# Optimization experiments

Hardware: AMD Instinct MI355X
Metric: run time of the kernel (lower is better)

Reference implementation:

```python
import jax, jax.numpy as jnp
import numpy as np

N = 8192   # points
C = 64     # feature planes (planes[0])
H = 4      # num_heads
K = 16     # nsample (KNN neighbors)
DH = C // H
EPS = 1e-9


def setup_inputs() -> dict:
    key = jax.random.key(0)
    ks = jax.random.split(key, 13)
    w = lambda k, sh: jax.random.normal(k, sh, jnp.float32) * 0.05
    p = jax.random.normal(ks[0], (N, 3), jnp.float32)
    nrm = jax.random.normal(ks[1], (N, 3), jnp.float32)
    normals = nrm / jnp.sqrt(jnp.sum(nrm * nrm, -1, keepdims=True) + EPS)
    x = jax.random.normal(ks[2], (N, C), jnp.float32)
    return {
        "p": p, "x": x, "normals": normals,
        "Wq": w(ks[3], (C, C)), "Wk": w(ks[4], (C, C)), "Wv": w(ks[5], (C, C)),
        "Wo": w(ks[6], (C, C)),
        "ppf_w1": w(ks[7], (4, C)), "ppf_b1": jnp.zeros((C,), jnp.float32),
        "ppf_w2": w(ks[8], (C, C)), "ppf_b2": jnp.zeros((C,), jnp.float32),
        "ln_g": jnp.ones((C,), jnp.float32), "ln_b": jnp.zeros((C,), jnp.float32),
    }


def _angle(u, v):
    # rotation-invariant angle via atan2(||u x v||, u . v); eps keeps grads finite at 0
    cr = jnp.cross(u, v)
    return jnp.arctan2(jnp.sqrt(jnp.sum(cr * cr, -1) + EPS), jnp.sum(u * v, -1))


def reference(p, x, normals, Wq, Wk, Wv, Wo, ppf_w1, ppf_b1, ppf_w2, ppf_b2, ln_g, ln_b):
    # --- KNN grouping (pointops.queryandgroup equivalent) ---
    sq = jnp.sum(p * p, -1)
    d2 = sq[:, None] + sq[None, :] - 2.0 * (p @ p.T)   # (N,N) pairwise sq dists
    _, idx = jax.lax.top_k(-d2, K)                      # (N,K) neighbor indices

    # --- PPF features (calc_ppf_gpu) ---
    p_r = p[idx]                                        # (N,K,3)
    n_r = normals[idx]                                  # (N,K,3)
    d = p_r - p[:, None, :]
    nc = jnp.broadcast_to(normals[:, None, :], d.shape)
    ppf = jnp.stack([
        _angle(nc, d),
        _angle(n_r, d),
        _angle(nc, n_r),
        jnp.sqrt(jnp.sum(d * d, -1) + EPS),
    ], -1)                                              # (N,K,4)

    # --- LocalPPFTransformer: PPF-conditioned local multi-head attention ---
    pe = jax.nn.relu(ppf @ ppf_w1 + ppf_b1) @ ppf_w2 + ppf_b2   # (N,K,C)
    q = (x @ Wq).reshape(N, H, DH)
    xg = x[idx]                                                  # (N,K,C) gather
    k = (xg @ Wk + pe).reshape(N, K, H, DH)
    v = (xg @ Wv + pe).reshape(N, K, H, DH)
    scale = 1.0 / np.sqrt(DH).astype(np.float32)
    attn = jax.nn.softmax(jnp.einsum('nhd,nkhd->nhk', q, k) * scale, axis=-1)
    out = jnp.einsum('nhk,nkhd->nhd', attn, v).reshape(N, C) @ Wo

    # --- block tail: LayerNorm, residual, ReLU ---
    mu = jnp.mean(out, -1, keepdims=True)
    var = jnp.var(out, -1, keepdims=True)
    out = (out - mu) * jax.lax.rsqrt(var + 1e-5) * ln_g + ln_b
    return jax.nn.relu(out + x)
```

## Files before the change

kernel.cpp:

```cpp
#include <hip/hip_runtime.h>
#include <hip/hip_bf16.h>
#include <math.h>

#define N_PTS 8192
#define QPW 4
#define LCAP 192
#define KNN_BLOCKS (N_PTS / 4)

#define OFF_W2 0
#define OFF_WO 4096
#define OFF_WQB 8192
#define OFF_WKB 12288
#define OFF_WVB 16384
#define PACK_N 20480
#define PREP_BLOCKS (N_PTS / 256)
#define PACK_BLOCKS ((PACK_N + 255) / 256)

typedef __hip_bfloat16 bf16;
typedef __attribute__((ext_vector_type(8))) short short8;
typedef __attribute__((ext_vector_type(4))) float floatx4;

#define INFF __int_as_float(0x7f800000)

__device__ __forceinline__ float ldf(const float* p, int i) { return p[i]; }
__device__ __forceinline__ float ldf(const bf16* p, int i) { return __bfloat162float(p[i]); }
__device__ __forceinline__ void stf(float* p, int i, float v) { p[i] = v; }
__device__ __forceinline__ void stf(bf16* p, int i, float v) { p[i] = __float2bfloat16(v); }

__device__ __forceinline__ unsigned short f2bfbits(float x) {
    bf16 h = __float2bfloat16(x);
    return *reinterpret_cast<unsigned short*>(&h);
}
__device__ __forceinline__ float bfbits2f(unsigned short u) {
    bf16 h;
    *reinterpret_cast<unsigned short*>(&h) = u;
    return __bfloat162float(h);
}

__device__ __forceinline__ short8 load_xfrag(const bf16* x, int row, int off) {
    return *(const short8*)((const unsigned short*)x + row * 64 + off);
}
__device__ __forceinline__ short8 load_xfrag(const float* x, int row, int off) {
    short8 v;
#pragma unroll
    for (int i = 0; i < 8; ++i) v[i] = (short)f2bfbits(x[row * 64 + off + i]);
    return v;
}

__device__ __forceinline__ bool is_bf16(const void* g) {
    return *(const unsigned int*)g != 0x3F800000u;
}

template <typename T>
__device__ __forceinline__ void prep_pack_body(const T* p, float4* p4,
                                               const T* w2, const T* Wo,
                                               const T* Wq, const T* Wk,
                                               const T* Wv,
                                               unsigned short* pack) {
    if (blockIdx.x < PREP_BLOCKS) {
        int i = blockIdx.x * 256 + threadIdx.x;
        float x = ldf(p, 3 * i + 0);
        float y = ldf(p, 3 * i + 1);
        float z = ldf(p, 3 * i + 2);
        p4[i] = make_float4(x, y, z, 0.5f * (x * x + y * y + z * z));
        return;
    }
    int i = (blockIdx.x - PREP_BLOCKS) * 256 + threadIdx.x;
    if (i >= PACK_N) return;
    if (i >= OFF_WO && i < OFF_WQB) {
        int j = i - OFF_WO, t = j >> 6, c = j & 63;
        pack[i] = f2bfbits(ldf(Wo, c * 64 + t));
    } else {
        const T* W = (i < OFF_WO) ? w2
                     : (i < OFF_WKB ? Wq : (i < OFF_WVB ? Wk : Wv));
        int j = i & 4095;
        int ii = j & 7, lane = (j >> 3) & 63, frag = j >> 9;
        int tile = frag >> 1, s = frag & 1, g = lane >> 4, m16 = lane & 15;
        int k = s * 32 + g * 8 + ii, n = tile * 16 + m16;
        pack[i] = f2bfbits(ldf(W, k * 64 + n));
    }
}
__global__ __launch_bounds__(256) void prep_pack_kernel(
    const void* p, float4* p4, const void* w2, const void* Wo, const void* Wq,
    const void* Wk, const void* Wv, unsigned short* pack, const void* gref) {
    if (is_bf16(gref))
        prep_pack_body<bf16>((const bf16*)p, p4, (const bf16*)w2,
                             (const bf16*)Wo, (const bf16*)Wq, (const bf16*)Wk,
                             (const bf16*)Wv, pack);
    else
        prep_pack_body<float>((const float*)p, p4, (const float*)w2,
                              (const float*)Wo, (const float*)Wq,
                              (const float*)Wk, (const float*)Wv, pack);
}

__device__ __forceinline__ float angle3(float ux, float uy, float uz, float vx,
                                        float vy, float vz) {
    float cx = uy * vz - uz * vy;
    float cy = uz * vx - ux * vz;
    float cz = ux * vy - uy * vx;
    float cn = sqrtf(cx * cx + cy * cy + cz * cz + 1e-9f);
    float d = ux * vx + uy * vy + uz * vz;
    return atan2f(cn, d);
}

template <typename T>
__device__ __forceinline__ void attn4_body(
    int n, int t, const float4* p4, const T* normals, const T* w1, const T* b1,
    const T* b2, const unsigned short* pack, const T* x, const T* ln_g,
    const T* ln_b, T* out, const int* nbr, float* scr,
    unsigned short (*kh)[72], unsigned short (*vbuf)[72]) {
    const int m16 = t & 15, g = t >> 4;

    float w10 = ldf(w1, 0 * 64 + t);
    float w11 = ldf(w1, 1 * 64 + t);
    float w12 = ldf(w1, 2 * 64 + t);
    float w13 = ldf(w1, 3 * 64 + t);
    float bb1 = ldf(b1, t);
    float b2c[4];
#pragma unroll
    for (int tile = 0; tile < 4; ++tile) b2c[tile] = ldf(b2, tile * 16 + m16);

    {
        int k = t >> 2, f = t & 3;
        int j = nbr[k];
        float4 pc = p4[n];
        float4 pj = p4[j];
        float dx = pj.x - pc.x, dy = pj.y - pc.y, dz = pj.z - pc.z;
        float v;
        if (f == 3) {
            v = sqrtf(dx * dx + dy * dy + dz * dz + 1e-9f);
        } else if (f == 0) {
            float ncx = ldf(normals, n * 3 + 0);
            float ncy = ldf(normals, n * 3 + 1);
            float ncz = ldf(normals, n * 3 + 2);
            v = angle3(ncx, ncy, ncz, dx, dy, dz);
        } else if (f == 1) {
            float njx = ldf(normals, j * 3 + 0);
            float njy = ldf(normals, j * 3 + 1);
            float njz = ldf(normals, j * 3 + 2);
            v = angle3(njx, njy, njz, dx, dy, dz);
        } else {
            float ncx = ldf(normals, n * 3 + 0);
            float ncy = ldf(normals, n * 3 + 1);
            float ncz = ldf(normals, n * 3 + 2);
            float njx = ldf(normals, j * 3 + 0);
            float njy = ldf(normals, j * 3 + 1);
            float njz = ldf(normals, j * 3 + 2);
            v = angle3(ncx, ncy, ncz, njx, njy, njz);
        }
        scr[t] = v;
    }
    __syncthreads();

    {
        const float4* pp = (const float4*)scr;
#pragma unroll
        for (int k = 0; k < 16; ++k) {
            float4 pf = pp[k];
            float h = fmaf(pf.w, w13,
                      fmaf(pf.z, w12, fmaf(pf.y, w11, fmaf(pf.x, w10, bb1))));
            kh[k][t] = f2bfbits(fmaxf(h, 0.0f));
        }
    }
    __syncthreads();

    short8 afr[2];
#pragma unroll
    for (int s = 0; s < 2; ++s)
        afr[s] = *(const short8*)&kh[m16][g * 8 + s * 32];

    short8 axfr[2], qfr[2];
#pragma unroll
    for (int s = 0; s < 2; ++s) {
        axfr[s] = load_xfrag(x, nbr[m16], g * 8 + s * 32);
        qfr[s] = load_xfrag(x, n, g * 8 + s * 32);
    }

    float qreg = 0.f;
    {
        const short8* pw2 = (const short8*)(pack + OFF_W2);
        const short8* pwq = (const short8*)(pack + OFF_WQB);
        const short8* pwk = (const short8*)(pack + OFF_WKB);
        const short8* pwv = (const short8*)(pack + OFF_WVB);
#pragma unroll
        for (int tile = 0; tile < 4; ++tile) {
            floatx4 accp = (floatx4){0.f, 0.f, 0.f, 0.f};
            accp = __builtin_amdgcn_mfma_f32_16x16x32_bf16(
                afr[0], pw2[(tile * 2 + 0) * 64 + t], accp, 0, 0, 0);
            accp = __builtin_amdgcn_mfma_f32_16x16x32_bf16(
                afr[1], pw2[(tile * 2 + 1) * 64 + t], accp, 0, 0, 0);
            floatx4 acck = accp;
            acck = __builtin_amdgcn_mfma_f32_16x16x32_bf16(
                axfr[0], pwk[(tile * 2 + 0) * 64 + t], acck, 0, 0, 0);
            acck = __builtin_amdgcn_mfma_f32_16x16x32_bf16(
                axfr[1], pwk[(tile * 2 + 1) * 64 + t], acck, 0, 0, 0);
            floatx4 accv = accp;
            accv = __builtin_amdgcn_mfma_f32_16x16x32_bf16(
                axfr[0], pwv[(tile * 2 + 0) * 64 + t], accv, 0, 0, 0);
            accv = __builtin_amdgcn_mfma_f32_16x16x32_bf16(
                axfr[1], pwv[(tile * 2 + 1) * 64 + t], accv, 0, 0, 0);
            floatx4 accq = (floatx4){0.f, 0.f, 0.f, 0.f};
            accq = __builtin_amdgcn_mfma_f32_16x16x32_bf16(
                qfr[0], pwq[(tile * 2 + 0) * 64 + t], accq, 0, 0, 0);
            accq = __builtin_amdgcn_mfma_f32_16x16x32_bf16(
                qfr[1], pwq[(tile * 2 + 1) * 64 + t], accq, 0, 0, 0);
            if (tile == g) qreg = accq[0];
#pragma unroll
            for (int r = 0; r < 4; ++r) {
                kh[g * 4 + r][tile * 16 + m16] =
                    f2bfbits(acck[r] + b2c[tile]);
                vbuf[g * 4 + r][tile * 16 + m16] =
                    f2bfbits(accv[r] + b2c[tile]);
            }
        }
    }
    __syncthreads();

    int h = t >> 4, kk = t & 15;
    float s = 0.f;
    {
        const short8* kv = (const short8*)&kh[kk][h * 16];
        short8 k0 = kv[0], k1 = kv[1];
        int qb = t & 0x30;
#pragma unroll
        for (int i = 0; i < 8; ++i)
            s = fmaf(__shfl(qreg, qb + i, 64),
                     bfbits2f((unsigned short)k0[i]), s);
#pragma unroll
        for (int i = 0; i < 8; ++i)
            s = fmaf(__shfl(qreg, qb + 8 + i, 64),
                     bfbits2f((unsigned short)k1[i]), s);
    }
    s *= 0.25f;

    float m = s;
#pragma unroll
    for (int off = 1; off < 16; off <<= 1)
        m = fmaxf(m, __shfl_xor(m, off, 16));
    float e = expf(s - m);
    float sum = e;
#pragma unroll
    for (int off = 1; off < 16; off <<= 1) sum += __shfl_xor(sum, off, 16);
    scr[t] = e / sum;
    __syncthreads();

    int hh = t >> 4;
    float o = 0.f;
    {
        const float4* aw = (const float4*)&scr[hh * 16];
#pragma unroll
        for (int j = 0; j < 4; ++j) {
            float4 a = aw[j];
            o = fmaf(a.x, bfbits2f(vbuf[j * 4 + 0][t]), o);
            o = fmaf(a.y, bfbits2f(vbuf[j * 4 + 1][t]), o);
            o = fmaf(a.z, bfbits2f(vbuf[j * 4 + 2][t]), o);
            o = fmaf(a.w, bfbits2f(vbuf[j * 4 + 3][t]), o);
        }
    }
    __syncthreads();
    scr[t] = o;
    __syncthreads();

    float wo = 0.f;
    {
        const short8* wo8 = (const short8*)(pack + OFF_WO) + t * 8;
        const float4* av = (const float4*)scr;
#pragma unroll
        for (int c8 = 0; c8 < 8; ++c8) {
            short8 w = wo8[c8];
            float4 a0 = av[c8 * 2 + 0], a1 = av[c8 * 2 + 1];
            wo = fmaf(a0.x, bfbits2f((unsigned short)w[0]), wo);
            wo = fmaf(a0.y, bfbits2f((unsigned short)w[1]), wo);
            wo = fmaf(a0.z, bfbits2f((unsigned short)w[2]), wo);
            wo = fmaf(a0.w, bfbits2f((unsigned short)w[3]), wo);
            wo = fmaf(a1.x, bfbits2f((unsigned short)w[4]), wo);
            wo = fmaf(a1.y, bfbits2f((unsigned short)w[5]), wo);
            wo = fmaf(a1.z, bfbits2f((unsigned short)w[6]), wo);
            wo = fmaf(a1.w, bfbits2f((unsigned short)w[7]), wo);
        }
    }

    float sum2 = wo;
#pragma unroll
    for (int off = 1; off < 64; off <<= 1) sum2 += __shfl_xor(sum2, off, 64);
    float mu = sum2 * (1.0f / 64.0f);
    float dc = wo - mu;
    float vs = dc * dc;
#pragma unroll
    for (int off = 1; off < 64; off <<= 1) vs += __shfl_xor(vs, off, 64);
    float var = vs * (1.0f / 64.0f);

    float y = dc * rsqrtf(var + 1e-5f) * ldf(ln_g, t) + ldf(ln_b, t);
    float r = y + ldf(x, n * 64 + t);
    stf(out, n * 64 + t, fmaxf(r, 0.0f));
}

union KnnAttnOverlay {
    struct {
        unsigned long long list[QPW][LCAP];
        float Tw[QPW][4];
        unsigned int cnt[QPW];
        int nbrs[4][16];
    } n;
    unsigned short vbuf[4][16][72];
};

__global__ __launch_bounds__(256, 8) void knn_attn_kernel(
    const float4* __restrict__ p4, const void* normals, const void* w1,
    const void* b1, const void* b2, const unsigned short* __restrict__ pack,
    const void* x, const void* ln_g, const void* ln_b, void* out) {
    __shared__ __align__(16) unsigned short kh4[4][16][72];
    __shared__ __align__(16) KnnAttnOverlay ov;
    __shared__ __align__(16) float scratch4[4][64];

    const int tid = threadIdx.x;
    const int lane = tid & 63;
    const int wave = tid >> 6;
    const int qbase = blockIdx.x * QPW;
    const int cbase = wave * (N_PTS / 4);

    float4 c[QPW];
#pragma unroll
    for (int q = 0; q < QPW; ++q) c[q] = p4[qbase + q];

    if (tid < QPW) ov.n.cnt[tid] = 0;

    float lmin[QPW];
#pragma unroll
    for (int q = 0; q < QPW; ++q) lmin[q] = INFF;

#pragma unroll 2
    for (int it = 0; it < N_PTS / 4 / 64; ++it) {
        float4 pj = p4[cbase + it * 64 + lane];
#pragma unroll
        for (int q = 0; q < QPW; ++q) {
            float f = fmaf(-c[q].x, pj.x,
                      fmaf(-c[q].y, pj.y, fmaf(-c[q].z, pj.z, pj.w)));
            lmin[q] = fminf(lmin[q], f);
        }
    }

#pragma unroll
    for (int q = 0; q < QPW; ++q) {
        float v = lmin[q];
#pragma unroll
        for (int k = 2; k <= 64; k <<= 1) {
#pragma unroll
            for (int j = k >> 1; j >= 1; j >>= 1) {
                float o = __shfl_xor(v, j, 64);
                bool keepmin = (((lane & k) == 0) == ((lane & j) == 0));
                v = keepmin ? fminf(v, o) : fmaxf(v, o);
            }
        }
        float Tw = __shfl(v, 15, 64);
        if (lane == 0) ov.n.Tw[q][wave] = Tw;
    }
    __syncthreads();

    float T[QPW];
#pragma unroll
    for (int q = 0; q < QPW; ++q)
        T[q] = fminf(fminf(ov.n.Tw[q][0], ov.n.Tw[q][1]),
                     fminf(ov.n.Tw[q][2], ov.n.Tw[q][3]));

#pragma unroll 2
    for (int it = 0; it < N_PTS / 4 / 64; ++it) {
        int j = cbase + it * 64 + lane;
        float4 pj = p4[j];
#pragma unroll
        for (int q = 0; q < QPW; ++q) {
            float f = fmaf(-c[q].x, pj.x,
                      fmaf(-c[q].y, pj.y, fmaf(-c[q].z, pj.z, pj.w)));
            bool sel = f <= T[q];
            unsigned long long ball = __ballot(sel);
            if (ball) {
                int leader = (int)__ffsll((long long)ball) - 1;
                unsigned int base = 0;
                if (lane == leader)
                    base = atomicAdd(&ov.n.cnt[q], (unsigned int)__popcll(ball));
                base = (unsigned int)__shfl((int)base, leader, 64);
                if (sel) {
                    unsigned int bits = __float_as_uint(f);
                    bits ^= (unsigned int)(((int)bits >> 31)) | 0x80000000u;
                    unsigned long long key =
                        ((unsigned long long)bits << 32) | (unsigned int)j;
                    unsigned int mb =
                        __builtin_amdgcn_mbcnt_lo((unsigned int)ball, 0u);
                    mb = __builtin_amdgcn_mbcnt_hi((unsigned int)(ball >> 32),
                                                   mb);
                    unsigned int pos = base + mb;
                    if (pos < LCAP) ov.n.list[q][pos] = key;
                }
            }
        }
    }
    __syncthreads();

    {
        const int q = wave;
        int m = ov.n.cnt[q] < (unsigned)LCAP ? (int)ov.n.cnt[q] : LCAP;
#pragma unroll
        for (int s = 0; s < LCAP / 64; ++s) {
            int idx = lane + s * 64;
            if (idx < m) {
                unsigned long long k = ov.n.list[q][idx];
                int r = 0;
#pragma unroll 1
                for (int e = 0; e < m; ++e) r += (ov.n.list[q][e] < k);
                if (r < 16) ov.n.nbrs[q][r] = (int)(k & 0xFFFFFFFFu);
            }
        }
    }
    __syncthreads();

    int n = qbase + wave;
    if (is_bf16(ln_g))
        attn4_body<bf16>(n, lane, p4, (const bf16*)normals, (const bf16*)w1,
                         (const bf16*)b1, (const bf16*)b2, pack,
                         (const bf16*)x, (const bf16*)ln_g, (const bf16*)ln_b,
                         (bf16*)out, ov.n.nbrs[wave], scratch4[wave],
                         kh4[wave], ov.vbuf[wave]);
    else
        attn4_body<float>(n, lane, p4, (const float*)normals, (const float*)w1,
                          (const float*)b1, (const float*)b2, pack,
                          (const float*)x, (const float*)ln_g,
                          (const float*)ln_b, (float*)out, ov.n.nbrs[wave],
                          scratch4[wave], kh4[wave], ov.vbuf[wave]);
}

extern "C" void kernel_launch(void* const* d_in, const int* in_sizes, int n_in,
                              void* d_out, int out_size, void* d_ws, size_t ws_size,
                              hipStream_t stream) {
    const void* p   = d_in[0];
    const void* x   = d_in[1];
    const void* nrm = d_in[2];
    const void* Wq  = d_in[3];
    const void* Wk  = d_in[4];
    const void* Wv  = d_in[5];
    const void* Wo  = d_in[6];
    const void* w1  = d_in[7];
    const void* b1  = d_in[8];
    const void* w2  = d_in[9];
    const void* b2  = d_in[10];
    const void* g   = d_in[11];
    const void* b   = d_in[12];

    char* ws = (char*)d_ws;
    float4* p4 = (float4*)ws;  ws += (size_t)N_PTS * sizeof(float4);
    unsigned short* pack = (unsigned short*)ws;  ws += PACK_N * 2;

    prep_pack_kernel<<<PREP_BLOCKS + PACK_BLOCKS, 256, 0, stream>>>(
        p, p4, w2, Wo, Wq, Wk, Wv, pack, g);
    knn_attn_kernel<<<KNN_BLOCKS, 256, 0, stream>>>(p4, nrm, w1, b1, b2, pack,
                                                    x, g, b, d_out);
}
```

Measured before the change: 149.0 us.

## Split fused KNN+attention kernel into separate KNN and attention kernels

Splits the fused kernel into a KNN kernel that writes 16-bit neighbor indices to workspace and a separate attention kernel that reads them. Each kernel can then be compiled and scheduled on its own, with its own register and LDS use, instead of carrying the worst case of both phases. The first KNN scan loop is also unrolled more. In exchange this adds a kernel launch and a global round trip for the index array, and gives up the LDS overlay that let vbuf share space with the KNN list.

New measurement: 155.7 us. 1.05x slower.

```diff
diff --git a/kernel.cpp b/kernel.cpp
--- a/kernel.cpp
+++ b/kernel.cpp
@@ -93,6 +93,118 @@
                               (const float*)Wk, (const float*)Wv, pack);
 }
 
+__global__ __launch_bounds__(256, 8) void knn_kernel(
+    const float4* __restrict__ p4, unsigned short* __restrict__ nbrs_g) {
+    __shared__ unsigned long long list[QPW][LCAP];
+    __shared__ float Tw_sh[QPW][4];
+    __shared__ unsigned int cnt[QPW];
+    __shared__ int nbrs[QPW][16];
+
+    const int tid = threadIdx.x;
+    const int lane = tid & 63;
+    const int wave = tid >> 6;
+    const int qbase = blockIdx.x * QPW;
+    const int cbase = wave * (N_PTS / 4);
+
+    float4 c[QPW];
+#pragma unroll
+    for (int q = 0; q < QPW; ++q) c[q] = p4[qbase + q];
+
+    if (tid < QPW) cnt[tid] = 0;
+
+    float lmin[QPW];
+#pragma unroll
+    for (int q = 0; q < QPW; ++q) lmin[q] = INFF;
+
+#pragma unroll 4
+    for (int it = 0; it < N_PTS / 4 / 64; ++it) {
+        float4 pj = p4[cbase + it * 64 + lane];
+#pragma unroll
+        for (int q = 0; q < QPW; ++q) {
+            float f = fmaf(-c[q].x, pj.x,
+                      fmaf(-c[q].y, pj.y, fmaf(-c[q].z, pj.z, pj.w)));
+            lmin[q] = fminf(lmin[q], f);
+        }
+    }
+
+#pragma unroll
+    for (int q = 0; q < QPW; ++q) {
+        float v = lmin[q];
+#pragma unroll
+        for (int k = 2; k <= 64; k <<= 1) {
+#pragma unroll
+            for (int j = k >> 1; j >= 1; j >>= 1) {
+                float o = __shfl_xor(v, j, 64);
+                bool keepmin = (((lane & k) == 0) == ((lane & j) == 0));
+                v = keepmin ? fminf(v, o) : fmaxf(v, o);
+            }
+        }
+        float Tw = __shfl(v, 15, 64);
+        if (lane == 0) Tw_sh[q][wave] = Tw;
+    }
+    __syncthreads();
+
+    float T[QPW];
+#pragma unroll
+    for (int q = 0; q < QPW; ++q)
+        T[q] = fminf(fminf(Tw_sh[q][0], Tw_sh[q][1]),
+                     fminf(Tw_sh[q][2], Tw_sh[q][3]));
+
+#pragma unroll 2
+    for (int it = 0; it < N_PTS / 4 / 64; ++it) {
+        int j = cbase + it * 64 + lane;
+        float4 pj = p4[j];
+#pragma unroll
+        for (int q = 0; q < QPW; ++q) {
+            float f = fmaf(-c[q].x, pj.x,
+                      fmaf(-c[q].y, pj.y, fmaf(-c[q].z, pj.z, pj.w)));
+            bool sel = f <= T[q];
+            unsigned long long ball = __ballot(sel);
+            if (ball) {
+                int leader = (int)__ffsll((long long)ball) - 1;
+                unsigned int base = 0;
+                if (lane == leader)
+                    base = atomicAdd(&cnt[q], (unsigned int)__popcll(ball));
+                base = (unsigned int)__shfl((int)base, leader, 64);
+                if (sel) {
+                    unsigned int bits = __float_as_uint(f);
+                    bits ^= (unsigned int)(((int)bits >> 31)) | 0x80000000u;
+                    unsigned long long key =
+                        ((unsigned long long)bits << 32) | (unsigned int)j;
+                    unsigned int mb =
+                        __builtin_amdgcn_mbcnt_lo((unsigned int)ball, 0u);
+                    mb = __builtin_amdgcn_mbcnt_hi((unsigned int)(ball >> 32),
+                                                   mb);
+                    unsigned int pos = base + mb;
+                    if (pos < LCAP) list[q][pos] = key;
+                }
+            }
+        }
+    }
+    __syncthreads();
+
+    {
+        const int q = wave;
+        int m = cnt[q] < (unsigned)LCAP ? (int)cnt[q] : LCAP;
+#pragma unroll
+        for (int s = 0; s < LCAP / 64; ++s) {
+            int idx = lane + s * 64;
+            if (idx < m) {
+                unsigned long long k = list[q][idx];
+                int r = 0;
+#pragma unroll 1
+                for (int e = 0; e < m; ++e) r += (list[q][e] < k);
+                if (r < 16) nbrs[q][r] = (int)(k & 0xFFFFFFFFu);
+            }
+        }
+    }
+    __syncthreads();
+
+    if (tid < QPW * 16)
+        nbrs_g[qbase * 16 + tid] =
+            (unsigned short)((const int*)nbrs)[tid];
+}
+
 __device__ __forceinline__ float angle3(float ux, float uy, float uz, float vx,
                                         float vy, float vz) {
     float cx = uy * vz - uz * vy;
@@ -107,7 +219,7 @@
 __device__ __forceinline__ void attn4_body(
     int n, int t, const float4* p4, const T* normals, const T* w1, const T* b1,
     const T* b2, const unsigned short* pack, const T* x, const T* ln_g,
-    const T* ln_b, T* out, const int* nbr, float* scr,
+    const T* ln_b, T* out, const unsigned short* nbr, float* scr,
     unsigned short (*kh)[72], unsigned short (*vbuf)[72]) {
     const int m16 = t & 15, g = t >> 4;
 
@@ -295,137 +407,32 @@
     stf(out, n * 64 + t, fmaxf(r, 0.0f));
 }
 
-union KnnAttnOverlay {
-    struct {
-        unsigned long long list[QPW][LCAP];
-        float Tw[QPW][4];
-        unsigned int cnt[QPW];
-        int nbrs[4][16];
-    } n;
-    unsigned short vbuf[4][16][72];
-};
-
-__global__ __launch_bounds__(256, 8) void knn_attn_kernel(
+__global__ __launch_bounds__(256, 8) void attn_kernel(
     const float4* __restrict__ p4, const void* normals, const void* w1,
     const void* b1, const void* b2, const unsigned short* __restrict__ pack,
-    const void* x, const void* ln_g, const void* ln_b, void* out) {
+    const void* x, const void* ln_g, const void* ln_b,
+    const unsigned short* __restrict__ nbrs_g, void* out) {
     __shared__ __align__(16) unsigned short kh4[4][16][72];
-    __shared__ __align__(16) KnnAttnOverlay ov;
+    __shared__ __align__(16) unsigned short vbuf4[4][16][72];
     __shared__ __align__(16) float scratch4[4][64];
 
-    const int tid = threadIdx.x;
-    const int lane = tid & 63;
-    const int wave = tid >> 6;
-    const int qbase = blockIdx.x * QPW;
-    const int cbase = wave * (N_PTS / 4);
-
-    float4 c[QPW];
-#pragma unroll
-    for (int q = 0; q < QPW; ++q) c[q] = p4[qbase + q];
-
-    if (tid < QPW) ov.n.cnt[tid] = 0;
-
-    float lmin[QPW];
-#pragma unroll
-    for (int q = 0; q < QPW; ++q) lmin[q] = INFF;
-
-#pragma unroll 2
-    for (int it = 0; it < N_PTS / 4 / 64; ++it) {
-        float4 pj = p4[cbase + it * 64 + lane];
-#pragma unroll
-        for (int q = 0; q < QPW; ++q) {
-            float f = fmaf(-c[q].x, pj.x,
-                      fmaf(-c[q].y, pj.y, fmaf(-c[q].z, pj.z, pj.w)));
-            lmin[q] = fminf(lmin[q], f);
-        }
-    }
-
-#pragma unroll
-    for (int q = 0; q < QPW; ++q) {
-        float v = lmin[q];
-#pragma unroll
-        for (int k = 2; k <= 64; k <<= 1) {
-#pragma unroll
-            for (int j = k >> 1; j >= 1; j >>= 1) {
-                float o = __shfl_xor(v, j, 64);
-                bool keepmin = (((lane & k) == 0) == ((lane & j) == 0));
-                v = keepmin ? fminf(v, o) : fmaxf(v, o);
-            }
-        }
-        float Tw = __shfl(v, 15, 64);
-        if (lane == 0) ov.n.Tw[q][wave] = Tw;
-    }
-    __syncthreads();
-
-    float T[QPW];
-#pragma unroll
-    for (int q = 0; q < QPW; ++q)
-        T[q] = fminf(fminf(ov.n.Tw[q][0], ov.n.Tw[q][1]),
-                     fminf(ov.n.Tw[q][2], ov.n.Tw[q][3]));
-
-#pragma unroll 2
-    for (int it = 0; it < N_PTS / 4 / 64; ++it) {
-        int j = cbase + it * 64 + lane;
-        float4 pj = p4[j];
-#pragma unroll
-        for (int q = 0; q < QPW; ++q) {
-            float f = fmaf(-c[q].x, pj.x,
-                      fmaf(-c[q].y, pj.y, fmaf(-c[q].z, pj.z, pj.w)));
-            bool sel = f <= T[q];
-            unsigned long long ball = __ballot(sel);
-            if (ball) {
-                int leader = (int)__ffsll((long long)ball) - 1;
-                unsigned int base = 0;
-                if (lane == leader)
-                    base = atomicAdd(&ov.n.cnt[q], (unsigned int)__popcll(ball));
-                base = (unsigned int)__shfl((int)base, leader, 64);
-                if (sel) {
-                    unsigned int bits = __float_as_uint(f);
-                    bits ^= (unsigned int)(((int)bits >> 31)) | 0x80000000u;
-                    unsigned long long key =
-                        ((unsigned long long)bits << 32) | (unsigned int)j;
-                    unsigned int mb =
-                        __builtin_amdgcn_mbcnt_lo((unsigned int)ball, 0u);
-                    mb = __builtin_amdgcn_mbcnt_hi((unsigned int)(ball >> 32),
-                                                   mb);
-                    unsigned int pos = base + mb;
-                    if (pos < LCAP) ov.n.list[q][pos] = key;
-                }
-            }
-        }
-    }
-    __syncthreads();
-
-    {
-        const int q = wave;
-        int m = ov.n.cnt[q] < (unsigned)LCAP ? (int)ov.n.cnt[q] : LCAP;
-#pragma unroll
-        for (int s = 0; s < LCAP / 64; ++s) {
-            int idx = lane + s * 64;
-            if (idx < m) {
-                unsigned long long k = ov.n.list[q][idx];
-                int r = 0;
-#pragma unroll 1
-                for (int e = 0; e < m; ++e) r += (ov.n.list[q][e] < k);
-                if (r < 16) ov.n.nbrs[q][r] = (int)(k & 0xFFFFFFFFu);
-            }
-        }
-    }
-    __syncthreads();
-
-    int n = qbase + wave;
+    const int lane = threadIdx.x & 63;
+    const int wave = threadIdx.x >> 6;
+    const int n = blockIdx.x * QPW + wave;
+    const unsigned short* nbr = nbrs_g + n * 16;
+
     if (is_bf16(ln_g))
         attn4_body<bf16>(n, lane, p4, (const bf16*)normals, (const bf16*)w1,
                          (const bf16*)b1, (const bf16*)b2, pack,
                          (const bf16*)x, (const bf16*)ln_g, (const bf16*)ln_b,
-                         (bf16*)out, ov.n.nbrs[wave], scratch4[wave],
-                         kh4[wave], ov.vbuf[wave]);
+                         (bf16*)out, nbr, scratch4[wave], kh4[wave],
+                         vbuf4[wave]);
     else
         attn4_body<float>(n, lane, p4, (const float*)normals, (const float*)w1,
                           (const float*)b1, (const float*)b2, pack,
                           (const float*)x, (const float*)ln_g,
-                          (const float*)ln_b, (float*)out, ov.n.nbrs[wave],
-                          scratch4[wave], kh4[wave], ov.vbuf[wave]);
+                          (const float*)ln_b, (float*)out, nbr,
+                          scratch4[wave], kh4[wave], vbuf4[wave]);
 }
 
 extern "C" void kernel_launch(void* const* d_in, const int* in_sizes, int n_in,
@@ -448,9 +455,11 @@
     char* ws = (char*)d_ws;
     float4* p4 = (float4*)ws;  ws += (size_t)N_PTS * sizeof(float4);
     unsigned short* pack = (unsigned short*)ws;  ws += PACK_N * 2;
+    unsigned short* nbrs_g = (unsigned short*)ws;  ws += (size_t)N_PTS * 16 * 2;
 
     prep_pack_kernel<<<PREP_BLOCKS + PACK_BLOCKS, 256, 0, stream>>>(
         p, p4, w2, Wo, Wq, Wk, Wv, pack, g);
-    knn_attn_kernel<<<KNN_BLOCKS, 256, 0, stream>>>(p4, nrm, w1, b1, b2, pack,
-                                                    x, g, b, d_out);
-}
+    knn_kernel<<<KNN_BLOCKS, 256, 0, stream>>>(p4, nbrs_g);
+    attn_kernel<<<KNN_BLOCKS, 256, 0, stream>>>(p4, nrm, w1, b1, b2, pack, x,
+                                                g, b, nbrs_g, d_out);
+}
```
